# Kernel optimization log

Hardware: AMD Instinct MI355X
Metric: run time of the kernel (lower is better)

The kernel has to match this reference:

```python
import jax, jax.numpy as jnp
import numpy as np

B, S, D, H = 2, 2048, 768, 12
Dh = D // H  # attention_head_size = 64
NEG = -1e9


def setup_inputs() -> dict:
    key = jax.random.key(0)
    ks = jax.random.split(key, 10)
    scale = 1.0 / np.sqrt(D).astype(np.float32)
    inp = {
        "hidden_states": jax.random.normal(ks[0], (B, S, D), jnp.float32),
        "Wq": jax.random.normal(ks[1], (D, D), jnp.float32) * scale,
        "bq": jnp.zeros((D,), jnp.float32),
        "Wk": jax.random.normal(ks[2], (D, D), jnp.float32) * scale,
        "bk": jnp.zeros((D,), jnp.float32),
        "Wv": jax.random.normal(ks[3], (D, D), jnp.float32) * scale,
        "bv": jnp.zeros((D,), jnp.float32),
        "Wo": jax.random.normal(ks[4], (D, D), jnp.float32) * scale,
        "bo": jnp.zeros((D,), jnp.float32),
        "mask": jax.random.randint(ks[5], (B, S), 0, 2).astype(bool),
    }
    return inp


def _heads(x):
    # [B,S,D] -> [B,H,S,Dh]
    return x.reshape(B, S, H, Dh).transpose(0, 2, 1, 3)


def reference(hidden_states, Wq, bq, Wk, bk, Wv, bv, Wo, bo, mask):
    q = _heads(hidden_states @ Wq + bq)
    k = _heads(hidden_states @ Wk + bk)
    v = _heads(hidden_states @ Wv + bv)

    # [B,H,S,S] raw scores
    scores = jnp.einsum("bhqd,bhkd->bhqk", q, k) / np.sqrt(Dh).astype(np.float32)

    # pairwise fg mask: [B,1,S,S]; True where both query and key tokens are fg
    am = mask[:, None, :, None] & mask[:, None, None, :]

    # fg softmax: bg pairs masked to -1e9; bg softmax: fg pairs masked to -1e9
    fg_probs = jax.nn.softmax(jnp.where(am, scores, NEG), axis=-1)
    bg_probs = jnp.where(am, NEG, scores)
    bg_probs = jax.nn.softmax(bg_probs, axis=-1)

    # stitch: take fg probs at fg pairs, bg probs elsewhere (replaces boolean scatter)
    probs = jnp.where(am, fg_probs, bg_probs)

    ctx = jnp.einsum("bhqk,bhkd->bhqd", probs, v)
    ctx = ctx.transpose(0, 2, 1, 3).reshape(B, S, D)
    return ctx @ Wo + bo
```

## Files before the change

kernel.cpp:

```cpp
#include <hip/hip_runtime.h>

typedef float f32x4 __attribute__((ext_vector_type(4)));
typedef short bf16x8 __attribute__((ext_vector_type(8)));

#define MFMA16(a, b, c) __builtin_amdgcn_mfma_f32_16x16x32_bf16((a), (b), (c), 0, 0, 0)

constexpr int S_ = 2048;
constexpr int D_ = 768;
constexpr int H_ = 12;
constexpr int DH = 64;
constexpr int B_ = 2;
constexpr int M_ = B_ * S_;
constexpr int BH = B_ * H_;

typedef unsigned short u16;
typedef unsigned int u32;

__device__ __forceinline__ u16 f2bf(float f) {
  u32 u = __builtin_bit_cast(u32, f);
  u += 0x7fffu + ((u >> 16) & 1u);
  return (u16)(u >> 16);
}
__device__ __forceinline__ u32 pack2(float a, float b) {
  return (u32)f2bf(a) | ((u32)f2bf(b) << 16);
}
__device__ __forceinline__ u32 pack2r(float lo, float hi) {
  u32 a = __builtin_bit_cast(u32, lo) + 0x8000u;
  u32 b = __builtin_bit_cast(u32, hi) + 0x8000u;
  return __builtin_amdgcn_perm(b, a, 0x07060302u);
}

__device__ __forceinline__ void gload16(const void* g, void* l) {
  __builtin_amdgcn_global_load_lds((const __attribute__((address_space(1))) u32*)g,
                                   (__attribute__((address_space(3))) u32*)l, 16, 0, 0);
}

__global__ __launch_bounds__(256) void conv_bf16(const float* __restrict__ in,
                                                 u16* __restrict__ out) {
  int i = blockIdx.x * 256 + threadIdx.x;
  float4 v = ((const float4*)in)[i];
  uint2 r;
  r.x = pack2(v.x, v.y);
  r.y = pack2(v.z, v.w);
  ((uint2*)out)[i] = r;
}

struct WPtrs {
  const float* s0; const float* s1; const float* s2; const float* s3;
  u16* d0; u16* d1; u16* d2; u16* d3;
};
__global__ __launch_bounds__(256) void conv_wT4(WPtrs p) {
  __shared__ float t[32][33];
  int z = blockIdx.z;
  const float* w = z == 0 ? p.s0 : z == 1 ? p.s1 : z == 2 ? p.s2 : p.s3;
  u16* wt = z == 0 ? p.d0 : z == 1 ? p.d1 : z == 2 ? p.d2 : p.d3;
  int k0 = blockIdx.x << 5, n0 = blockIdx.y << 5;
  int x = threadIdx.x & 31, y = threadIdx.x >> 5;
#pragma unroll
  for (int j = 0; j < 4; ++j) t[y + 8 * j][x] = w[(size_t)(k0 + y + 8 * j) * D_ + n0 + x];
  __syncthreads();
#pragma unroll
  for (int j = 0; j < 4; ++j) wt[(size_t)(n0 + y + 8 * j) * D_ + k0 + x] = f2bf(t[x][y + 8 * j]);
}

__global__ __launch_bounds__(256) void canon_mask(const void* __restrict__ mraw,
                                                  float* __restrict__ fm,
                                                  u32* __restrict__ mw) {
  __shared__ int isBool;
  int tid = threadIdx.x;
  if (tid == 0) isBool = 0;
  __syncthreads();
  const int* mi = (const int*)mraw;
  int v = mi[tid];
  if (v != 0 && v != 1) atomicOr(&isBool, 1);
  __syncthreads();
  const unsigned char* mb = (const unsigned char*)mraw;
  int p = blockIdx.x * 256 + tid;
  int m0, m1;
  if (isBool) { m0 = mb[2 * p]; m1 = mb[2 * p + 1]; }
  else        { m0 = mi[2 * p]; m1 = mi[2 * p + 1]; }
  fm[2 * p] = (float)m0;
  fm[2 * p + 1] = (float)m1;
  mw[p] = (m0 ? 0xFFFFu : 0u) | (m1 ? 0xFFFF0000u : 0u);
}

template <int MODE>
__global__ __launch_bounds__(256) void gemm64(const u16* __restrict__ A,
                                              const u16* __restrict__ Wt,
                                              const float* __restrict__ bias,
                                              void* __restrict__ outp, float scale) {
  __shared__ __align__(16) u16 lA[2][64 * 64];
  __shared__ __align__(16) u16 lB[2][64 * 64];
  int tid = threadIdx.x;
  int w = tid >> 6, lane = tid & 63, g = lane >> 4, c = lane & 15;
  int m0 = blockIdx.x * 64, n0 = blockIdx.y * 64;
  int srow = lane >> 3;
  int scb = ((lane & 7) * 16) ^ (srow << 4);
  int sw = (c & 7) << 4;
  const char* Ab = (const char*)A + (size_t)m0 * (D_ * 2);
  const char* Bb = (const char*)Wt + (size_t)n0 * (D_ * 2);

  auto stage = [&](int buf, int k0) {
    int r0 = w * 16 + srow, r1 = w * 16 + 8 + srow;
    gload16(Ab + (size_t)r0 * (D_ * 2) + k0 * 2 + scb, &lA[buf][(w * 16) * 64]);
    gload16(Ab + (size_t)r1 * (D_ * 2) + k0 * 2 + scb, &lA[buf][(w * 16 + 8) * 64]);
    gload16(Bb + (size_t)r0 * (D_ * 2) + k0 * 2 + scb, &lB[buf][(w * 16) * 64]);
    gload16(Bb + (size_t)r1 * (D_ * 2) + k0 * 2 + scb, &lB[buf][(w * 16 + 8) * 64]);
  };

  f32x4 acc[4] = {};
  stage(0, 0);
  __syncthreads();
  int buf = 0;
  for (int t = 0; t < D_ / 64; ++t) {
    if (t + 1 < D_ / 64) stage(buf ^ 1, (t + 1) * 64);
    const char* pa = (const char*)&lA[buf][0];
    const char* pb = (const char*)&lB[buf][0];
#pragma unroll
    for (int kk = 0; kk < 2; ++kk) {
      int cs = (kk * 64 + g * 16) ^ sw;
      bf16x8 af = *(const bf16x8*)(pa + (w * 16 + c) * 128 + cs);
#pragma unroll
      for (int j = 0; j < 4; ++j) {
        bf16x8 bfj = *(const bf16x8*)(pb + (j * 16 + c) * 128 + cs);
        acc[j] = MFMA16(af, bfj, acc[j]);
      }
    }
    __syncthreads();
    buf ^= 1;
  }

#pragma unroll
  for (int j = 0; j < 4; ++j) {
    int n = n0 + j * 16 + c;
    float bv = bias[n];
    int h = n >> 6, d = n & 63;
    if (MODE == 1) {
      int m = m0 + w * 16 + g * 4;
      int b = m >> 11, s = m & (S_ - 1);
      int chunk = s >> 5, kq = (s >> 2) & 7;
      int sb = kq < 4 ? 8 * kq : 8 * (kq - 4) + 4;
      float v0 = acc[j][0] + bv, v1 = acc[j][1] + bv;
      float v2 = acc[j][2] + bv, v3 = acc[j][3] + bv;
      uint2 pk;
      pk.x = pack2r(v0, v1);
      pk.y = pack2r(v2, v3);
      u16* dst = (u16*)outp + ((size_t)((b * H_ + h) * DH + d)) * S_ + chunk * 32 + sb;
      *(uint2*)dst = pk;
    } else {
#pragma unroll
      for (int r = 0; r < 4; ++r) {
        int m = m0 + w * 16 + g * 4 + r;
        float v = (acc[j][r] + bv) * scale;
        if (MODE == 0) {
          int b = m >> 11, s = m & (S_ - 1);
          ((u16*)outp)[((size_t)(b * H_ + h) * S_ + s) * DH + d] = f2bf(v);
        } else {
          ((float*)outp)[(size_t)m * D_ + n] = v;
        }
      }
    }
  }
}

__global__ __launch_bounds__(256, 3) void attn(const u16* __restrict__ Q,
                                               const u16* __restrict__ K,
                                               const u16* __restrict__ Vt,
                                               const float* __restrict__ fm,
                                               const u32* __restrict__ mw,
                                               u16* __restrict__ ctx) {
  constexpr int NT = S_ / 64;
  __shared__ __align__(16) u16 lK[2][64 * 64];
  __shared__ __align__(16) u16 lV[2][64 * 64];

  const int tid = threadIdx.x;
  const int w = tid >> 6, lane = tid & 63;
  const int g = lane >> 4, c = lane & 15;
  const int qt = blockIdx.x, bh = blockIdx.y;
  const int b = bh / H_, h = bh % H_;
  const int qbase = qt * 64;

  const u16* Qp = Q + ((size_t)bh * S_ + qbase + w * 16) * DH;
  const char* Kp = (const char*)(K + (size_t)bh * S_ * DH);
  const char* Vp = (const char*)(Vt + (size_t)bh * DH * S_);
  const float* fmp = fm + b * S_;
  const u32* mwp = mw + b * (S_ / 2);

  bf16x8 qf0 = *(const bf16x8*)(Qp + c * DH + g * 8);
  bf16x8 qf1 = *(const bf16x8*)(Qp + c * DH + 32 + g * 8);

  u32 ow = (c == 0) ? 0x3F803F80u : 0u;
  uint4 owv = {ow, ow, ow, ow};
  bf16x8 onesf = __builtin_bit_cast(bf16x8, owv);

  const int srow = lane >> 3;
  const int scb = ((lane & 7) * 16) ^ (srow << 4);
  const int r8a = w * 2, r8b = w * 2 + 1;
  const int rowA = r8a * 8 + srow, rowB = r8b * 8 + srow;
  const int sw = (c & 7) << 4;

  f32x4 accf[4] = {}, accb[4] = {}, alf = {}, alb = {};

  gload16(Kp + (size_t)rowA * 128 + scb, &lK[0][r8a * 512]);
  gload16(Kp + (size_t)rowB * 128 + scb, &lK[0][r8b * 512]);
  gload16(Vp + (size_t)rowA * 4096 + scb, &lV[0][r8a * 512]);
  gload16(Vp + (size_t)rowB * 4096 + scb, &lV[0][r8b * 512]);
  __syncthreads();

  int buf = 0;
  for (int t = 0; t < NT; ++t) {
    if (t + 1 < NT) {
      const char* kb_ = Kp + (size_t)(t + 1) * 8192;
      const char* vb_ = Vp + (size_t)(t + 1) * 128;
      gload16(kb_ + (size_t)rowA * 128 + scb, &lK[buf ^ 1][r8a * 512]);
      gload16(kb_ + (size_t)rowB * 128 + scb, &lK[buf ^ 1][r8b * 512]);
      gload16(vb_ + (size_t)rowA * 4096 + scb, &lV[buf ^ 1][r8a * 512]);
      gload16(vb_ + (size_t)rowB * 4096 + scb, &lV[buf ^ 1][r8b * 512]);
    }
    const char* kt = (const char*)&lK[buf][0];
    const char* vtl = (const char*)&lV[buf][0];

#pragma unroll
    for (int kc = 0; kc < 2; ++kc) {
      const int csel = (kc * 64 + g * 16) ^ sw;
      bf16x8 k00 = *(const bf16x8*)(kt + (kc * 32 + c) * 128 + ((g * 16) ^ sw));
      bf16x8 k01 = *(const bf16x8*)(kt + (kc * 32 + c) * 128 + ((64 + g * 16) ^ sw));
      bf16x8 k10 = *(const bf16x8*)(kt + (kc * 32 + 16 + c) * 128 + ((g * 16) ^ sw));
      bf16x8 k11 = *(const bf16x8*)(kt + (kc * 32 + 16 + c) * 128 + ((64 + g * 16) ^ sw));

      f32x4 st0 = {}, st1 = {};
      st0 = MFMA16(k00, qf0, st0);
      st0 = MFMA16(k01, qf1, st0);
      st1 = MFMA16(k10, qf0, st1);
      st1 = MFMA16(k11, qf1, st1);

      u32 ew0 = pack2r(__builtin_amdgcn_exp2f(st0[0]), __builtin_amdgcn_exp2f(st0[1]));
      u32 ew1 = pack2r(__builtin_amdgcn_exp2f(st0[2]), __builtin_amdgcn_exp2f(st0[3]));
      u32 ew2 = pack2r(__builtin_amdgcn_exp2f(st1[0]), __builtin_amdgcn_exp2f(st1[1]));
      u32 ew3 = pack2r(__builtin_amdgcn_exp2f(st1[2]), __builtin_amdgcn_exp2f(st1[3]));

      const int pbase = ((t * 64 + kc * 32) >> 1);
      uint2 m01 = *(const uint2*)(mwp + pbase + 2 * g);
      uint2 m23 = *(const uint2*)(mwp + pbase + 8 + 2 * g);

      u32 pf0 = ew0 & m01.x, pf1 = ew1 & m01.y;
      u32 pf2 = ew2 & m23.x, pf3 = ew3 & m23.y;
      uint4 pfv = {pf0, pf1, pf2, pf3};
      uint4 pbv = {ew0 ^ pf0, ew1 ^ pf1, ew2 ^ pf2, ew3 ^ pf3};
      bf16x8 paf = __builtin_bit_cast(bf16x8, pfv);
      bf16x8 pab = __builtin_bit_cast(bf16x8, pbv);

      bf16x8 vf0 = *(const bf16x8*)(vtl + (0 * 16 + c) * 128 + csel);
      bf16x8 vf1 = *(const bf16x8*)(vtl + (1 * 16 + c) * 128 + csel);
      bf16x8 vf2 = *(const bf16x8*)(vtl + (2 * 16 + c) * 128 + csel);
      bf16x8 vf3 = *(const bf16x8*)(vtl + (3 * 16 + c) * 128 + csel);

      accf[0] = MFMA16(paf, vf0, accf[0]);
      accb[0] = MFMA16(pab, vf0, accb[0]);
      accf[1] = MFMA16(paf, vf1, accf[1]);
      accb[1] = MFMA16(pab, vf1, accb[1]);
      accf[2] = MFMA16(paf, vf2, accf[2]);
      accb[2] = MFMA16(pab, vf2, accb[2]);
      accf[3] = MFMA16(paf, vf3, accf[3]);
      accb[3] = MFMA16(pab, vf3, accb[3]);
      alf = MFMA16(paf, onesf, alf);
      alb = MFMA16(pab, onesf, alb);
    }
    __syncthreads();
    buf ^= 1;
  }

  const int qw = qbase + w * 16;
#pragma unroll
  for (int r = 0; r < 4; ++r) {
    int ql = g * 4 + r;
    float lfr = __shfl(alf[r], g * 16);
    float lbr = __shfl(alb[r], g * 16);
    bool fg = fmp[qw + ql] > 0.5f;
    float inv_f = (lfr > 0.f) ? 1.f / lfr : 0.f;
    float inv_b = (lbr > 0.f) ? 1.f / lbr : 0.f;
    float inv_all = 1.f / (lfr + lbr);
#pragma unroll
    for (int n = 0; n < 4; ++n) {
      float o = fg ? (accf[n][r] * inv_f + accb[n][r] * inv_b)
                   : ((accf[n][r] + accb[n][r]) * inv_all);
      ctx[((size_t)(b * S_ + qw + ql)) * D_ + h * DH + n * 16 + c] = f2bf(o);
    }
  }
}

extern "C" void kernel_launch(void* const* d_in, const int* in_sizes, int n_in,
                              void* d_out, int out_size, void* d_ws, size_t ws_size,
                              hipStream_t stream) {
  const float* hs = (const float*)d_in[0];
  const float* Wq = (const float*)d_in[1];
  const float* bq = (const float*)d_in[2];
  const float* Wk = (const float*)d_in[3];
  const float* bk = (const float*)d_in[4];
  const float* Wv = (const float*)d_in[5];
  const float* bv = (const float*)d_in[6];
  const float* Wo = (const float*)d_in[7];
  const float* bo = (const float*)d_in[8];
  const void* mraw = d_in[9];

  char* ws = (char*)d_ws;
  size_t off = 0;
  auto alloc = [&](size_t bytes) {
    void* p = ws + off;
    off += (bytes + 255) & ~(size_t)255;
    return p;
  };
  u16* hsb = (u16*)alloc((size_t)M_ * D_ * 2);
  u16* wqT = (u16*)alloc((size_t)D_ * D_ * 2);
  u16* wkT = (u16*)alloc((size_t)D_ * D_ * 2);
  u16* wvT = (u16*)alloc((size_t)D_ * D_ * 2);
  u16* woT = (u16*)alloc((size_t)D_ * D_ * 2);
  u16* qb = (u16*)alloc((size_t)M_ * D_ * 2);
  u16* kb = (u16*)alloc((size_t)M_ * D_ * 2);
  u16* vtb = (u16*)alloc((size_t)M_ * D_ * 2);
  u16* ctx = (u16*)alloc((size_t)M_ * D_ * 2);
  float* fmf = (float*)alloc((size_t)B_ * S_ * 4);
  u32* mwb = (u32*)alloc((size_t)B_ * S_ / 2 * 4);

  conv_bf16<<<(M_ * D_ / 4 + 255) / 256, 256, 0, stream>>>(hs, hsb);
  WPtrs wp = {Wq, Wk, Wv, Wo, wqT, wkT, wvT, woT};
  conv_wT4<<<dim3(D_ / 32, D_ / 32, 4), 256, 0, stream>>>(wp);
  canon_mask<<<B_ * S_ / 512, 256, 0, stream>>>(mraw, fmf, mwb);

  dim3 gg(M_ / 64, D_ / 64);
  const float qscale = 0.125f * 1.44269504088896f;
  gemm64<0><<<gg, 256, 0, stream>>>(hsb, wqT, bq, qb, qscale);
  gemm64<0><<<gg, 256, 0, stream>>>(hsb, wkT, bk, kb, 1.0f);
  gemm64<1><<<gg, 256, 0, stream>>>(hsb, wvT, bv, vtb, 1.0f);

  attn<<<dim3(S_ / 64, BH), 256, 0, stream>>>(qb, kb, vtb, fmf, mwb, ctx);

  gemm64<2><<<gg, 256, 0, stream>>>(ctx, woT, bo, d_out, 1.0f);
}
```

Before: 115.0 us.

## Fuse QKV GEMMs into one 128x128 tiled kernel and widen attention per-wave query tiles

The three Q/K/V projections become a single launch over a concatenated transposed weight, using 128x128 tiles where each wave computes a 64x64 block for more register reuse. The output projection uses the same kernel. Attention now runs 128-thread blocks in which each wave handles 32 queries, so every K/V fragment read from LDS feeds twice as much MFMA work. The mask words are staged once into LDS instead of being read from global memory in the inner loop, and s_setprio brackets the MFMA sequences. The aims are fewer launches and less LDS and global traffic per FLOP, at the cost of higher register pressure and fewer resident waves.

```diff
diff --git a/kernel.cpp b/kernel.cpp
--- a/kernel.cpp
+++ b/kernel.cpp
@@ -45,15 +45,16 @@
   ((uint2*)out)[i] = r;
 }
 
-struct WPtrs {
-  const float* s0; const float* s1; const float* s2; const float* s3;
-  u16* d0; u16* d1; u16* d2; u16* d3;
-};
-__global__ __launch_bounds__(256) void conv_wT4(WPtrs p) {
+__global__ __launch_bounds__(256) void conv_wT4(const float* __restrict__ Wq,
+                                                const float* __restrict__ Wk,
+                                                const float* __restrict__ Wv,
+                                                const float* __restrict__ Wo,
+                                                u16* __restrict__ wqkv,
+                                                u16* __restrict__ wo) {
   __shared__ float t[32][33];
   int z = blockIdx.z;
-  const float* w = z == 0 ? p.s0 : z == 1 ? p.s1 : z == 2 ? p.s2 : p.s3;
-  u16* wt = z == 0 ? p.d0 : z == 1 ? p.d1 : z == 2 ? p.d2 : p.d3;
+  const float* w = z == 0 ? Wq : z == 1 ? Wk : z == 2 ? Wv : Wo;
+  u16* wt = z == 3 ? wo : wqkv + (size_t)z * D_ * D_;
   int k0 = blockIdx.x << 5, n0 = blockIdx.y << 5;
   int x = threadIdx.x & 31, y = threadIdx.x >> 5;
 #pragma unroll
@@ -85,85 +86,116 @@
 }
 
 template <int MODE>
-__global__ __launch_bounds__(256) void gemm64(const u16* __restrict__ A,
-                                              const u16* __restrict__ Wt,
-                                              const float* __restrict__ bias,
-                                              void* __restrict__ outp, float scale) {
-  __shared__ __align__(16) u16 lA[2][64 * 64];
-  __shared__ __align__(16) u16 lB[2][64 * 64];
-  int tid = threadIdx.x;
-  int w = tid >> 6, lane = tid & 63, g = lane >> 4, c = lane & 15;
-  int m0 = blockIdx.x * 64, n0 = blockIdx.y * 64;
-  int srow = lane >> 3;
-  int scb = ((lane & 7) * 16) ^ (srow << 4);
-  int sw = (c & 7) << 4;
+__global__ __launch_bounds__(256, 2) void gemm128(const u16* __restrict__ A,
+                                                  const u16* __restrict__ Wt,
+                                                  const float* __restrict__ bq,
+                                                  const float* __restrict__ bk,
+                                                  const float* __restrict__ bv,
+                                                  u16* __restrict__ oq,
+                                                  u16* __restrict__ ok,
+                                                  u16* __restrict__ ov,
+                                                  float* __restrict__ of,
+                                                  float qscale) {
+  constexpr int NT = D_ / 64;
+  __shared__ __align__(16) u16 lA[2][128 * 64];
+  __shared__ __align__(16) u16 lB[2][128 * 64];
+  const int tid = threadIdx.x, w = tid >> 6, lane = tid & 63;
+  const int g = lane >> 4, c = lane & 15;
+  const int m0 = blockIdx.x * 128, n0 = blockIdx.y * 128;
+  const int wr = w >> 1, wc = w & 1;
+  const int srow = lane >> 3, scb = ((lane & 7) * 16) ^ (srow << 4);
+  const int sw = (c & 7) << 4;
   const char* Ab = (const char*)A + (size_t)m0 * (D_ * 2);
   const char* Bb = (const char*)Wt + (size_t)n0 * (D_ * 2);
 
-  auto stage = [&](int buf, int k0) {
-    int r0 = w * 16 + srow, r1 = w * 16 + 8 + srow;
-    gload16(Ab + (size_t)r0 * (D_ * 2) + k0 * 2 + scb, &lA[buf][(w * 16) * 64]);
-    gload16(Ab + (size_t)r1 * (D_ * 2) + k0 * 2 + scb, &lA[buf][(w * 16 + 8) * 64]);
-    gload16(Bb + (size_t)r0 * (D_ * 2) + k0 * 2 + scb, &lB[buf][(w * 16) * 64]);
-    gload16(Bb + (size_t)r1 * (D_ * 2) + k0 * 2 + scb, &lB[buf][(w * 16 + 8) * 64]);
-  };
-
-  f32x4 acc[4] = {};
-  stage(0, 0);
-  __syncthreads();
-  int buf = 0;
-  for (int t = 0; t < D_ / 64; ++t) {
-    if (t + 1 < D_ / 64) stage(buf ^ 1, (t + 1) * 64);
+  auto stage = [&](int buf, int t) {
+    int k0b = t * 128;
+#pragma unroll
+    for (int a = 0; a < 4; ++a) {
+      int rr = w * 32 + a * 8;
+      gload16(Ab + (size_t)(rr + srow) * (D_ * 2) + k0b + scb, &lA[buf][rr * 64]);
+      gload16(Bb + (size_t)(rr + srow) * (D_ * 2) + k0b + scb, &lB[buf][rr * 64]);
+    }
+  };
+
+  f32x4 acc[4][4] = {};
+  auto compute = [&](int buf) {
     const char* pa = (const char*)&lA[buf][0];
     const char* pb = (const char*)&lB[buf][0];
 #pragma unroll
     for (int kk = 0; kk < 2; ++kk) {
-      int cs = (kk * 64 + g * 16) ^ sw;
-      bf16x8 af = *(const bf16x8*)(pa + (w * 16 + c) * 128 + cs);
-#pragma unroll
-      for (int j = 0; j < 4; ++j) {
-        bf16x8 bfj = *(const bf16x8*)(pb + (j * 16 + c) * 128 + cs);
-        acc[j] = MFMA16(af, bfj, acc[j]);
-      }
-    }
+      const int cs = (kk * 64 + g * 16) ^ sw;
+      bf16x8 af[4], bf[4];
+#pragma unroll
+      for (int i = 0; i < 4; ++i)
+        af[i] = *(const bf16x8*)(pa + (wr * 64 + i * 16 + c) * 128 + cs);
+#pragma unroll
+      for (int j = 0; j < 4; ++j)
+        bf[j] = *(const bf16x8*)(pb + (wc * 64 + j * 16 + c) * 128 + cs);
+      __builtin_amdgcn_s_setprio(1);
+#pragma unroll
+      for (int i = 0; i < 4; ++i)
+#pragma unroll
+        for (int j = 0; j < 4; ++j) acc[i][j] = MFMA16(af[i], bf[j], acc[i][j]);
+      __builtin_amdgcn_s_setprio(0);
+    }
+  };
+
+  stage(0, 0);
+  __syncthreads();
+  int buf = 0;
+#pragma unroll 1
+  for (int t = 0; t < NT; ++t) {
+    if (t + 1 < NT) stage(buf ^ 1, t + 1);
+    compute(buf);
     __syncthreads();
     buf ^= 1;
   }
 
-#pragma unroll
-  for (int j = 0; j < 4; ++j) {
-    int n = n0 + j * 16 + c;
-    float bv = bias[n];
-    int h = n >> 6, d = n & 63;
-    if (MODE == 1) {
-      int m = m0 + w * 16 + g * 4;
-      int b = m >> 11, s = m & (S_ - 1);
-      int chunk = s >> 5, kq = (s >> 2) & 7;
-      int sb = kq < 4 ? 8 * kq : 8 * (kq - 4) + 4;
-      float v0 = acc[j][0] + bv, v1 = acc[j][1] + bv;
-      float v2 = acc[j][2] + bv, v3 = acc[j][3] + bv;
-      uint2 pk;
-      pk.x = pack2r(v0, v1);
-      pk.y = pack2r(v2, v3);
-      u16* dst = (u16*)outp + ((size_t)((b * H_ + h) * DH + d)) * S_ + chunk * 32 + sb;
-      *(uint2*)dst = pk;
-    } else {
-#pragma unroll
-      for (int r = 0; r < 4; ++r) {
-        int m = m0 + w * 16 + g * 4 + r;
-        float v = (acc[j][r] + bv) * scale;
-        if (MODE == 0) {
-          int b = m >> 11, s = m & (S_ - 1);
-          ((u16*)outp)[((size_t)(b * H_ + h) * S_ + s) * DH + d] = f2bf(v);
+  if (MODE == 0) {
+    const int p = n0 / D_;
+    const int nn0 = n0 - p * D_;
+    const float* bias = p == 0 ? bq : p == 1 ? bk : bv;
+    const float sc = p == 0 ? qscale : 1.0f;
+#pragma unroll
+    for (int j = 0; j < 4; ++j) {
+      int nn = nn0 + wc * 64 + j * 16 + c;
+      float bvv = bias[nn];
+      int h = nn >> 6, d = nn & 63;
+#pragma unroll
+      for (int i = 0; i < 4; ++i) {
+        int m = m0 + wr * 64 + i * 16 + g * 4;
+        int b = m >> 11, s = m & (S_ - 1);
+        if (p < 2) {
+          u16* dst = (p == 0 ? oq : ok) + ((size_t)(b * H_ + h) * S_ + s) * DH + d;
+#pragma unroll
+          for (int r = 0; r < 4; ++r) dst[(size_t)r * DH] = f2bf((acc[i][j][r] + bvv) * sc);
         } else {
-          ((float*)outp)[(size_t)m * D_ + n] = v;
+          int chunk = s >> 5, kq = (s >> 2) & 7;
+          int sb = kq < 4 ? 8 * kq : 8 * (kq - 4) + 4;
+          uint2 pk;
+          pk.x = pack2r(acc[i][j][0] + bvv, acc[i][j][1] + bvv);
+          pk.y = pack2r(acc[i][j][2] + bvv, acc[i][j][3] + bvv);
+          *(uint2*)(ov + ((size_t)((b * H_ + h) * DH + d)) * S_ + chunk * 32 + sb) = pk;
         }
       }
     }
+  } else {
+#pragma unroll
+    for (int j = 0; j < 4; ++j) {
+      int n = n0 + wc * 64 + j * 16 + c;
+      float bvv = bq[n];
+#pragma unroll
+      for (int i = 0; i < 4; ++i) {
+        int m = m0 + wr * 64 + i * 16 + g * 4;
+#pragma unroll
+        for (int r = 0; r < 4; ++r) of[(size_t)(m + r) * D_ + n] = acc[i][j][r] + bvv;
+      }
+    }
   }
 }
 
-__global__ __launch_bounds__(256, 3) void attn(const u16* __restrict__ Q,
+__global__ __launch_bounds__(128, 2) void attn(const u16* __restrict__ Q,
                                                const u16* __restrict__ K,
                                                const u16* __restrict__ Vt,
                                                const float* __restrict__ fm,
@@ -172,22 +204,27 @@
   constexpr int NT = S_ / 64;
   __shared__ __align__(16) u16 lK[2][64 * 64];
   __shared__ __align__(16) u16 lV[2][64 * 64];
+  __shared__ __align__(16) u32 lM[S_ / 2];
 
   const int tid = threadIdx.x;
   const int w = tid >> 6, lane = tid & 63;
   const int g = lane >> 4, c = lane & 15;
   const int qt = blockIdx.x, bh = blockIdx.y;
   const int b = bh / H_, h = bh % H_;
-  const int qbase = qt * 64;
-
-  const u16* Qp = Q + ((size_t)bh * S_ + qbase + w * 16) * DH;
+  const int qbase = qt * 64 + w * 32;
+
+  const u16* Qp = Q + ((size_t)bh * S_ + qbase) * DH;
   const char* Kp = (const char*)(K + (size_t)bh * S_ * DH);
   const char* Vp = (const char*)(Vt + (size_t)bh * DH * S_);
   const float* fmp = fm + b * S_;
-  const u32* mwp = mw + b * (S_ / 2);
-
-  bf16x8 qf0 = *(const bf16x8*)(Qp + c * DH + g * 8);
-  bf16x8 qf1 = *(const bf16x8*)(Qp + c * DH + 32 + g * 8);
+  const char* mwp = (const char*)(mw + b * (S_ / 2));
+
+  bf16x8 qf[2][2];
+#pragma unroll
+  for (int qs = 0; qs < 2; ++qs)
+#pragma unroll
+    for (int kk = 0; kk < 2; ++kk)
+      qf[qs][kk] = *(const bf16x8*)(Qp + (qs * 16 + c) * DH + kk * 32 + g * 8);
 
   u32 ow = (c == 0) ? 0x3F803F80u : 0u;
   uint4 owv = {ow, ow, ow, ow};
@@ -195,96 +232,104 @@
 
   const int srow = lane >> 3;
   const int scb = ((lane & 7) * 16) ^ (srow << 4);
-  const int r8a = w * 2, r8b = w * 2 + 1;
-  const int rowA = r8a * 8 + srow, rowB = r8b * 8 + srow;
   const int sw = (c & 7) << 4;
 
-  f32x4 accf[4] = {}, accb[4] = {}, alf = {}, alb = {};
-
-  gload16(Kp + (size_t)rowA * 128 + scb, &lK[0][r8a * 512]);
-  gload16(Kp + (size_t)rowB * 128 + scb, &lK[0][r8b * 512]);
-  gload16(Vp + (size_t)rowA * 4096 + scb, &lV[0][r8a * 512]);
-  gload16(Vp + (size_t)rowB * 4096 + scb, &lV[0][r8b * 512]);
-  __syncthreads();
-
-  int buf = 0;
-  for (int t = 0; t < NT; ++t) {
-    if (t + 1 < NT) {
-      const char* kb_ = Kp + (size_t)(t + 1) * 8192;
-      const char* vb_ = Vp + (size_t)(t + 1) * 128;
-      gload16(kb_ + (size_t)rowA * 128 + scb, &lK[buf ^ 1][r8a * 512]);
-      gload16(kb_ + (size_t)rowB * 128 + scb, &lK[buf ^ 1][r8b * 512]);
-      gload16(vb_ + (size_t)rowA * 4096 + scb, &lV[buf ^ 1][r8a * 512]);
-      gload16(vb_ + (size_t)rowB * 4096 + scb, &lV[buf ^ 1][r8b * 512]);
-    }
+  f32x4 accf[2][4] = {}, accb[2][4] = {}, alf[2] = {}, alb[2] = {};
+
+  auto stage = [&](int buf, int t) {
+    const char* kb_ = Kp + (size_t)t * 8192;
+    const char* vb_ = Vp + (size_t)t * 128;
+#pragma unroll
+    for (int a = 0; a < 4; ++a) {
+      int rr = w * 32 + a * 8;
+      gload16(kb_ + (size_t)(rr + srow) * 128 + scb, &lK[buf][rr * 64]);
+      gload16(vb_ + (size_t)(rr + srow) * 4096 + scb, &lV[buf][rr * 64]);
+    }
+  };
+
+  auto compute = [&](int buf, int t) {
     const char* kt = (const char*)&lK[buf][0];
     const char* vtl = (const char*)&lV[buf][0];
-
 #pragma unroll
     for (int kc = 0; kc < 2; ++kc) {
-      const int csel = (kc * 64 + g * 16) ^ sw;
+      uint2 m01 = *(const uint2*)((const char*)lM + t * 128 + kc * 64 + g * 8);
+      uint2 m23 = *(const uint2*)((const char*)lM + t * 128 + kc * 64 + 32 + g * 8);
       bf16x8 k00 = *(const bf16x8*)(kt + (kc * 32 + c) * 128 + ((g * 16) ^ sw));
       bf16x8 k01 = *(const bf16x8*)(kt + (kc * 32 + c) * 128 + ((64 + g * 16) ^ sw));
       bf16x8 k10 = *(const bf16x8*)(kt + (kc * 32 + 16 + c) * 128 + ((g * 16) ^ sw));
       bf16x8 k11 = *(const bf16x8*)(kt + (kc * 32 + 16 + c) * 128 + ((64 + g * 16) ^ sw));
-
-      f32x4 st0 = {}, st1 = {};
-      st0 = MFMA16(k00, qf0, st0);
-      st0 = MFMA16(k01, qf1, st0);
-      st1 = MFMA16(k10, qf0, st1);
-      st1 = MFMA16(k11, qf1, st1);
-
-      u32 ew0 = pack2r(__builtin_amdgcn_exp2f(st0[0]), __builtin_amdgcn_exp2f(st0[1]));
-      u32 ew1 = pack2r(__builtin_amdgcn_exp2f(st0[2]), __builtin_amdgcn_exp2f(st0[3]));
-      u32 ew2 = pack2r(__builtin_amdgcn_exp2f(st1[0]), __builtin_amdgcn_exp2f(st1[1]));
-      u32 ew3 = pack2r(__builtin_amdgcn_exp2f(st1[2]), __builtin_amdgcn_exp2f(st1[3]));
-
-      const int pbase = ((t * 64 + kc * 32) >> 1);
-      uint2 m01 = *(const uint2*)(mwp + pbase + 2 * g);
-      uint2 m23 = *(const uint2*)(mwp + pbase + 8 + 2 * g);
-
-      u32 pf0 = ew0 & m01.x, pf1 = ew1 & m01.y;
-      u32 pf2 = ew2 & m23.x, pf3 = ew3 & m23.y;
-      uint4 pfv = {pf0, pf1, pf2, pf3};
-      uint4 pbv = {ew0 ^ pf0, ew1 ^ pf1, ew2 ^ pf2, ew3 ^ pf3};
-      bf16x8 paf = __builtin_bit_cast(bf16x8, pfv);
-      bf16x8 pab = __builtin_bit_cast(bf16x8, pbv);
-
+      const int csel = (kc * 64 + g * 16) ^ sw;
       bf16x8 vf0 = *(const bf16x8*)(vtl + (0 * 16 + c) * 128 + csel);
       bf16x8 vf1 = *(const bf16x8*)(vtl + (1 * 16 + c) * 128 + csel);
       bf16x8 vf2 = *(const bf16x8*)(vtl + (2 * 16 + c) * 128 + csel);
       bf16x8 vf3 = *(const bf16x8*)(vtl + (3 * 16 + c) * 128 + csel);
-
-      accf[0] = MFMA16(paf, vf0, accf[0]);
-      accb[0] = MFMA16(pab, vf0, accb[0]);
-      accf[1] = MFMA16(paf, vf1, accf[1]);
-      accb[1] = MFMA16(pab, vf1, accb[1]);
-      accf[2] = MFMA16(paf, vf2, accf[2]);
-      accb[2] = MFMA16(pab, vf2, accb[2]);
-      accf[3] = MFMA16(paf, vf3, accf[3]);
-      accb[3] = MFMA16(pab, vf3, accb[3]);
-      alf = MFMA16(paf, onesf, alf);
-      alb = MFMA16(pab, onesf, alb);
-    }
+#pragma unroll
+      for (int qs = 0; qs < 2; ++qs) {
+        f32x4 st0 = {}, st1 = {};
+        __builtin_amdgcn_s_setprio(1);
+        st0 = MFMA16(k00, qf[qs][0], st0);
+        st0 = MFMA16(k01, qf[qs][1], st0);
+        st1 = MFMA16(k10, qf[qs][0], st1);
+        st1 = MFMA16(k11, qf[qs][1], st1);
+        __builtin_amdgcn_s_setprio(0);
+        u32 ew0 = pack2r(__builtin_amdgcn_exp2f(st0[0]), __builtin_amdgcn_exp2f(st0[1]));
+        u32 ew1 = pack2r(__builtin_amdgcn_exp2f(st0[2]), __builtin_amdgcn_exp2f(st0[3]));
+        u32 ew2 = pack2r(__builtin_amdgcn_exp2f(st1[0]), __builtin_amdgcn_exp2f(st1[1]));
+        u32 ew3 = pack2r(__builtin_amdgcn_exp2f(st1[2]), __builtin_amdgcn_exp2f(st1[3]));
+        u32 pf0 = ew0 & m01.x, pf1 = ew1 & m01.y;
+        u32 pf2 = ew2 & m23.x, pf3 = ew3 & m23.y;
+        uint4 pfv = {pf0, pf1, pf2, pf3};
+        uint4 pbv = {ew0 ^ pf0, ew1 ^ pf1, ew2 ^ pf2, ew3 ^ pf3};
+        bf16x8 paf = __builtin_bit_cast(bf16x8, pfv);
+        bf16x8 pab = __builtin_bit_cast(bf16x8, pbv);
+        __builtin_amdgcn_s_setprio(1);
+        accf[qs][0] = MFMA16(paf, vf0, accf[qs][0]);
+        accb[qs][0] = MFMA16(pab, vf0, accb[qs][0]);
+        accf[qs][1] = MFMA16(paf, vf1, accf[qs][1]);
+        accb[qs][1] = MFMA16(pab, vf1, accb[qs][1]);
+        accf[qs][2] = MFMA16(paf, vf2, accf[qs][2]);
+        accb[qs][2] = MFMA16(pab, vf2, accb[qs][2]);
+        accf[qs][3] = MFMA16(paf, vf3, accf[qs][3]);
+        accb[qs][3] = MFMA16(pab, vf3, accb[qs][3]);
+        alf[qs] = MFMA16(paf, onesf, alf[qs]);
+        alb[qs] = MFMA16(pab, onesf, alb[qs]);
+        __builtin_amdgcn_s_setprio(0);
+      }
+    }
+  };
+
+  gload16(mwp + w * 2048 + lane * 16, &lM[w * 512]);
+  gload16(mwp + w * 2048 + 1024 + lane * 16, &lM[w * 512 + 256]);
+  stage(0, 0);
+  __syncthreads();
+
+  int buf = 0;
+#pragma unroll 1
+  for (int t = 0; t < NT; ++t) {
+    if (t + 1 < NT) stage(buf ^ 1, t + 1);
+    compute(buf, t);
     __syncthreads();
     buf ^= 1;
   }
 
-  const int qw = qbase + w * 16;
-#pragma unroll
-  for (int r = 0; r < 4; ++r) {
-    int ql = g * 4 + r;
-    float lfr = __shfl(alf[r], g * 16);
-    float lbr = __shfl(alb[r], g * 16);
-    bool fg = fmp[qw + ql] > 0.5f;
-    float inv_f = (lfr > 0.f) ? 1.f / lfr : 0.f;
-    float inv_b = (lbr > 0.f) ? 1.f / lbr : 0.f;
-    float inv_all = 1.f / (lfr + lbr);
-#pragma unroll
-    for (int n = 0; n < 4; ++n) {
-      float o = fg ? (accf[n][r] * inv_f + accb[n][r] * inv_b)
-                   : ((accf[n][r] + accb[n][r]) * inv_all);
-      ctx[((size_t)(b * S_ + qw + ql)) * D_ + h * DH + n * 16 + c] = f2bf(o);
+#pragma unroll
+  for (int qs = 0; qs < 2; ++qs) {
+    const int qw = qbase + qs * 16;
+#pragma unroll
+    for (int r = 0; r < 4; ++r) {
+      int ql = g * 4 + r;
+      float lfr = __shfl(alf[qs][r], g * 16);
+      float lbr = __shfl(alb[qs][r], g * 16);
+      bool fg = fmp[qw + ql] > 0.5f;
+      float inv_f = (lfr > 0.f) ? 1.f / lfr : 0.f;
+      float inv_b = (lbr > 0.f) ? 1.f / lbr : 0.f;
+      float inv_all = 1.f / (lfr + lbr);
+#pragma unroll
+      for (int n = 0; n < 4; ++n) {
+        float o = fg ? (accf[qs][n][r] * inv_f + accb[qs][n][r] * inv_b)
+                     : ((accf[qs][n][r] + accb[qs][n][r]) * inv_all);
+        ctx[((size_t)(b * S_ + qw + ql)) * D_ + h * DH + n * 16 + c] = f2bf(o);
+      }
     }
   }
 }
@@ -311,9 +356,7 @@
     return p;
   };
   u16* hsb = (u16*)alloc((size_t)M_ * D_ * 2);
-  u16* wqT = (u16*)alloc((size_t)D_ * D_ * 2);
-  u16* wkT = (u16*)alloc((size_t)D_ * D_ * 2);
-  u16* wvT = (u16*)alloc((size_t)D_ * D_ * 2);
+  u16* wqkvT = (u16*)alloc((size_t)3 * D_ * D_ * 2);
   u16* woT = (u16*)alloc((size_t)D_ * D_ * 2);
   u16* qb = (u16*)alloc((size_t)M_ * D_ * 2);
   u16* kb = (u16*)alloc((size_t)M_ * D_ * 2);
@@ -323,17 +366,15 @@
   u32* mwb = (u32*)alloc((size_t)B_ * S_ / 2 * 4);
 
   conv_bf16<<<(M_ * D_ / 4 + 255) / 256, 256, 0, stream>>>(hs, hsb);
-  WPtrs wp = {Wq, Wk, Wv, Wo, wqT, wkT, wvT, woT};
-  conv_wT4<<<dim3(D_ / 32, D_ / 32, 4), 256, 0, stream>>>(wp);
+  conv_wT4<<<dim3(D_ / 32, D_ / 32, 4), 256, 0, stream>>>(Wq, Wk, Wv, Wo, wqkvT, woT);
   canon_mask<<<B_ * S_ / 512, 256, 0, stream>>>(mraw, fmf, mwb);
 
-  dim3 gg(M_ / 64, D_ / 64);
   const float qscale = 0.125f * 1.44269504088896f;
-  gemm64<0><<<gg, 256, 0, stream>>>(hsb, wqT, bq, qb, qscale);
-  gemm64<0><<<gg, 256, 0, stream>>>(hsb, wkT, bk, kb, 1.0f);
-  gemm64<1><<<gg, 256, 0, stream>>>(hsb, wvT, bv, vtb, 1.0f);
-
-  attn<<<dim3(S_ / 64, BH), 256, 0, stream>>>(qb, kb, vtb, fmf, mwb, ctx);
-
-  gemm64<2><<<gg, 256, 0, stream>>>(ctx, woT, bo, d_out, 1.0f);
-}
+  gemm128<0><<<dim3(M_ / 128, 3 * D_ / 128), 256, 0, stream>>>(
+      hsb, wqkvT, bq, bk, bv, qb, kb, vtb, nullptr, qscale);
+
+  attn<<<dim3(S_ / 64, BH), 128, 0, stream>>>(qb, kb, vtb, fmf, mwb, ctx);
+
+  gemm128<1><<<dim3(M_ / 128, D_ / 128), 256, 0, stream>>>(
+      ctx, woT, bo, nullptr, nullptr, nullptr, nullptr, nullptr, (float*)d_out, 1.0f);
+}
```

After: 118.3 us. 2.9% more time.
